# Kernel tuning notes

Hardware: AMD Instinct MI355X
Metric: run time of the kernel (lower is better)

Reference implementation:

```python
import jax, jax.numpy as jnp
import numpy as np
from math import pi

# Layer dims for num_inputs=0, width=64, depth=5, num_outputs=3
CHANNELS = [4, 64, 64, 64, 64, 3]

def _splits():
    biases, weights, idx = [], [], 0
    for l in range(len(CHANNELS) - 1):
        nci, nco = CHANNELS[l], CHANNELS[l + 1]
        biases.append((idx, idx + nco)); idx += nco
        weights.append((idx, idx + nci * nco)); idx += nci * nco
    return biases, weights, idx

BIASES, WEIGHTS, NUM_PARAMS = _splits()  # NUM_PARAMS == 12995


def _get_coords(h, w, ds):
    """Faithful port of _get_coords, including the original's bug where the
    y-channels reuse the normalized x coordinate vector (requires h == w)."""
    scale = 7.0 / 8.0
    x = jnp.arange(w, dtype=jnp.float32)
    y = jnp.arange(h, dtype=jnp.float32)
    x_c = (jnp.remainder(x, ds) / ds)
    y_c = (jnp.remainder(y, ds) / ds)
    x_c = x_c / (x_c.max() / scale)          # x_cos == x_sin in original
    y_cn = x_c / (y_c.max() / scale)          # bug: built from x_c
    xcos = jnp.cos(2.0 * pi * x_c)
    xsin = jnp.sin(2.0 * pi * x_c)
    ycos = jnp.cos(2.0 * pi * y_cn)           # length w, laid out along h (h==w)
    ysin = jnp.sin(2.0 * pi * y_cn)
    row = lambda v: jnp.broadcast_to(v[None, :], (h, w))
    col = lambda v: jnp.broadcast_to(v[:, None], (h, w))
    return jnp.stack([row(xcos), row(xsin), col(ycos), col(ysin)], axis=0)  # (4,h,w)


def setup_inputs() -> dict:
    key = jax.random.key(0)
    k1, k2 = jax.random.split(key)
    highres = jax.random.normal(k1, (2, 4, 512, 512), dtype=jnp.float32)
    lr_params = jax.random.normal(k2, (2, NUM_PARAMS, 64, 64), dtype=jnp.float32)
    return {"highres": highres, "lr_params": lr_params}


def reference(highres, lr_params):
    bs, _, h, w = highres.shape
    h_lr, w_lr = lr_params.shape[2], lr_params.shape[3]
    k = h // h_lr  # tile size

    coords = _get_coords(h, w, k)                       # (4, h, w)
    pe = jnp.broadcast_to(coords[None], (bs, 4, h, w))  # highres is overwritten by PE

    # unfold into (bs, h_lr, w_lr, k*k, 4) tiles
    tiles = pe.reshape(bs, 4, h_lr, k, w_lr, k)
    tiles = tiles.transpose(0, 2, 4, 3, 5, 1).reshape(bs, h_lr, w_lr, k * k, 4)

    out = tiles
    num_layers = len(CHANNELS) - 1
    for idx in range(num_layers):
        nci, nco = CHANNELS[idx], CHANNELS[idx + 1]
        b0, b1 = BIASES[idx]
        w0, w1 = WEIGHTS[idx]
        w_ = lr_params[:, w0:w1].transpose(0, 2, 3, 1).reshape(bs, h_lr, w_lr, nci, nco)
        b_ = lr_params[:, b0:b1].transpose(0, 2, 3, 1)[:, :, :, None, :]  # (bs,h_lr,w_lr,1,nco)
        out = jnp.einsum('bhwpi,bhwio->bhwpo', out, w_) + b_
        if idx < num_layers - 1:
            out = jnp.where(out >= 0, out, 0.01 * out)  # leaky_relu(0.01)
        else:
            out = jnp.tanh(out)

    out = out.reshape(bs, h_lr, w_lr, k, k, CHANNELS[-1])
    out = out.transpose(0, 5, 1, 3, 2, 4).reshape(bs, CHANNELS[-1], h, w)
    return out
```

## Files before the change

kernel.cpp:

```cpp
#include <hip/hip_runtime.h>
#include <math.h>


static constexpr int PLANE = 4096;
static constexpr int NPAR  = 12995;
static constexpr int AHI   = 8192;

__device__ __forceinline__ float leaky(float v) { return fmaxf(v, 0.01f * v); }

__device__ __forceinline__ constexpr float cx(int k) {
  constexpr float R = 0.70710678118654752f;
  const float t[8] = {1.f, R, 0.f, -R, -1.f, -R, 0.f, R};
  return t[k];
}
__device__ __forceinline__ constexpr float sx(int k) {
  constexpr float R = 0.70710678118654752f;
  const float t[8] = {0.f, R, 1.f, R, 0.f, -R, -1.f, -R};
  return t[k];
}

__global__ __launch_bounds__(256, 1) void pqn(const float* __restrict__ lr,
                                              float* __restrict__ out) {
  __shared__ alignas(16) float A[2 * AHI];
  __shared__ alignas(16) float WB[2][2048];

  const int tid = threadIdx.x;
  const int j   = tid & 3;
  const int pg  = (tid >> 2) & 7;
  const int cob = tid >> 5;

  const int n  = blockIdx.x;
  const int e2 = (n >> 3) & 3;
  const int P  = (n & 7) | ((n >> 5) << 3);
  const int jg = ((P & 3) << 2) | e2;
  const int i  = (P >> 2) & 63;
  const int b  = (P >> 8) & 1;

  const float* __restrict__ wb =
      lr + (size_t)b * NPAR * PLANE + (size_t)(i * 64 + jg * 4);
  const float* __restrict__ pt = wb + j;

  float fyc, fys;
  sincosf(0.78539816339744830962f * pg, &fys, &fyc);

  const int abase = pg * 16 + j * 4;
  const int swz   = j * 4;
  const int wr0   = (cob * 8) ^ swz;
  const int sq    = tid >> 7;
  const int sc    = tid & 127;

  auto gaddr = [&](int g) -> size_t {
    return 384 + (size_t)(g >> 3) * 4160 + (size_t)(g & 7) * 512;
  };

  float4 paA, paB, pbA, pbB;
  {
    const size_t cb = gaddr(0);
    paA = *(const float4*)(wb + (cb + tid) * PLANE);
    paB = *(const float4*)(wb + (cb + 256 + tid) * PLANE);
  }
  float l0b[8], l0w[32], bb[8];
#pragma unroll
  for (int m = 0; m < 8; ++m) l0b[m] = pt[(size_t)(cob * 8 + m) * PLANE];
#pragma unroll
  for (int f = 0; f < 4; ++f)
#pragma unroll
    for (int m = 0; m < 8; ++m)
      l0w[f * 8 + m] = pt[(size_t)(64 + f * 64 + cob * 8 + m) * PLANE];
#pragma unroll
  for (int m = 0; m < 8; ++m) bb[m] = pt[(size_t)(320 + cob * 8 + m) * PLANE];

#pragma unroll
  for (int col = 0; col < 8; ++col) {
    float t[8];
#pragma unroll
    for (int k = 0; k < 8; ++k) {
      float v = l0b[col];
      v = fmaf(cx(k), l0w[col], v);
      v = fmaf(sx(k), l0w[8 + col], v);
      v = fmaf(fyc,  l0w[16 + col], v);
      v = fmaf(fys,  l0w[24 + col], v);
      t[k] = leaky(v);
    }
    float4 v0, v1;
    v0.x = t[0]; v0.y = t[1]; v0.z = t[2]; v0.w = t[3];
    v1.x = t[4]; v1.y = t[5]; v1.z = t[6]; v1.w = t[7];
    *(float4*)&A[(cob * 8 + col) * 128 + abase]       = v0;
    *(float4*)&A[(cob * 8 + col) * 128 + abase + AHI] = v1;
  }
#pragma unroll
  for (int jj = 0; jj < 4; ++jj) {
    WB[0][sq * 512       + jj * 128 + (sc ^ (jj * 4))] = ((const float*)&paA)[jj];
    WB[0][(2 + sq) * 512 + jj * 128 + (sc ^ (jj * 4))] = ((const float*)&paB)[jj];
  }
  {
    size_t cb = gaddr(1);
    paA = *(const float4*)(wb + (cb + tid) * PLANE);
    paB = *(const float4*)(wb + (cb + 256 + tid) * PLANE);
    cb = gaddr(2);
    pbA = *(const float4*)(wb + (cb + tid) * PLANE);
    pbB = *(const float4*)(wb + (cb + 256 + tid) * PLANE);
  }
  asm volatile("s_waitcnt lgkmcnt(0)" ::: "memory");
  __builtin_amdgcn_s_barrier();
  __builtin_amdgcn_sched_barrier(0);

  float y[64];
#pragma unroll
  for (int m = 0; m < 64; ++m) y[m] = 0.f;

  auto cgrp = [&](int g, int h) {
    const int r0 = (g & 7) * 8;
#pragma unroll
    for (int q = 0; q < 4; ++q) {
      const float* Wt = &WB[h][q * 512 + j * 128];
#pragma unroll
      for (int cl = 0; cl < 2; ++cl) {
        const int ci = r0 + q * 2 + cl;
        const float4 a0 = *(const float4*)&A[ci * 128 + abase];
        const float4 a1 = *(const float4*)&A[ci * 128 + abase + AHI];
        const float4 w0 = *(const float4*)&Wt[(cl * 64) + wr0];
        const float4 w1 = *(const float4*)&Wt[((cl * 64 + cob * 8 + 4) ^ swz)];
        const float av[8] = {a0.x, a0.y, a0.z, a0.w, a1.x, a1.y, a1.z, a1.w};
        const float wv[8] = {w0.x, w0.y, w0.z, w0.w, w1.x, w1.y, w1.z, w1.w};
#pragma unroll
        for (int col = 0; col < 8; ++col)
#pragma unroll
          for (int k = 0; k < 8; ++k)
            y[col * 8 + k] = fmaf(av[k], wv[col], y[col * 8 + k]);
      }
    }
  };
  auto flush = [&](int l) {
#pragma unroll
    for (int col = 0; col < 8; ++col) {
      float4 v0, v1;
      v0.x = leaky(y[col * 8 + 0] + bb[col]);
      v0.y = leaky(y[col * 8 + 1] + bb[col]);
      v0.z = leaky(y[col * 8 + 2] + bb[col]);
      v0.w = leaky(y[col * 8 + 3] + bb[col]);
      v1.x = leaky(y[col * 8 + 4] + bb[col]);
      v1.y = leaky(y[col * 8 + 5] + bb[col]);
      v1.z = leaky(y[col * 8 + 6] + bb[col]);
      v1.w = leaky(y[col * 8 + 7] + bb[col]);
      *(float4*)&A[(cob * 8 + col) * 128 + abase]       = v0;
      *(float4*)&A[(cob * 8 + col) * 128 + abase + AHI] = v1;
    }
#pragma unroll
    for (int m = 0; m < 64; ++m) y[m] = 0.f;
    if (l < 2) {
#pragma unroll
      for (int m = 0; m < 8; ++m)
        bb[m] = pt[(size_t)(320 + (l + 1) * 4160 + cob * 8 + m) * PLANE];
    }
  };

#pragma unroll 1
  for (int u = 0; u < 12; ++u) {
    const int g0 = u * 2;
#pragma unroll
    for (int jj = 0; jj < 4; ++jj) {
      WB[1][sq * 512       + jj * 128 + (sc ^ (jj * 4))] = ((const float*)&paA)[jj];
      WB[1][(2 + sq) * 512 + jj * 128 + (sc ^ (jj * 4))] = ((const float*)&paB)[jj];
    }
    if (g0 + 3 < 24) {
      const size_t cb = gaddr(g0 + 3);
      paA = *(const float4*)(wb + (cb + tid) * PLANE);
      paB = *(const float4*)(wb + (cb + 256 + tid) * PLANE);
    }
    cgrp(g0, 0);
    asm volatile("s_waitcnt lgkmcnt(0)" ::: "memory");
    __builtin_amdgcn_s_barrier();
    __builtin_amdgcn_sched_barrier(0);

    const int g1 = g0 + 1;
    if (g1 + 1 < 24) {
#pragma unroll
      for (int jj = 0; jj < 4; ++jj) {
        WB[0][sq * 512       + jj * 128 + (sc ^ (jj * 4))] = ((const float*)&pbA)[jj];
        WB[0][(2 + sq) * 512 + jj * 128 + (sc ^ (jj * 4))] = ((const float*)&pbB)[jj];
      }
    }
    if (g1 + 3 < 24) {
      const size_t cb = gaddr(g1 + 3);
      pbA = *(const float4*)(wb + (cb + tid) * PLANE);
      pbB = *(const float4*)(wb + (cb + 256 + tid) * PLANE);
    }
    cgrp(g1, 1);
    asm volatile("s_waitcnt lgkmcnt(0)" ::: "memory");
    __builtin_amdgcn_s_barrier();
    __builtin_amdgcn_sched_barrier(0);
    if ((g1 & 7) == 7) {
      flush(g1 >> 3);
      asm volatile("s_waitcnt lgkmcnt(0)" ::: "memory");
      __builtin_amdgcn_s_barrier();
      __builtin_amdgcn_sched_barrier(0);
    }
  }

  float po[24];
#pragma unroll
  for (int m = 0; m < 24; ++m) po[m] = 0.f;
#pragma unroll
  for (int cl = 0; cl < 8; ++cl) {
    const int ci = cob * 8 + cl;
    const float4 a0 = *(const float4*)&A[ci * 128 + abase];
    const float4 a1 = *(const float4*)&A[ci * 128 + abase + AHI];
#pragma unroll
    for (int o = 0; o < 3; ++o) {
      const float w = pt[(size_t)(12803 + ci * 3 + o) * PLANE];
      po[o * 8 + 0] = fmaf(a0.x, w, po[o * 8 + 0]);
      po[o * 8 + 1] = fmaf(a0.y, w, po[o * 8 + 1]);
      po[o * 8 + 2] = fmaf(a0.z, w, po[o * 8 + 2]);
      po[o * 8 + 3] = fmaf(a0.w, w, po[o * 8 + 3]);
      po[o * 8 + 4] = fmaf(a1.x, w, po[o * 8 + 4]);
      po[o * 8 + 5] = fmaf(a1.y, w, po[o * 8 + 5]);
      po[o * 8 + 6] = fmaf(a1.z, w, po[o * 8 + 6]);
      po[o * 8 + 7] = fmaf(a1.w, w, po[o * 8 + 7]);
    }
  }
  asm volatile("s_waitcnt lgkmcnt(0)" ::: "memory");
  __builtin_amdgcn_s_barrier();
  float* R = A;
#pragma unroll
  for (int m = 0; m < 24; m += 4)
    *(float4*)&R[tid * 28 + m] = *(float4*)&po[m];
  asm volatile("s_waitcnt lgkmcnt(0)" ::: "memory");
  __builtin_amdgcn_s_barrier();
  __builtin_amdgcn_sched_barrier(0);

  if (cob == 0) {
#pragma unroll
    for (int o = 0; o < 3; ++o) {
      const float bias = pt[(size_t)(12800 + o) * PLANE];
      float s[8];
#pragma unroll
      for (int k = 0; k < 8; ++k) s[k] = bias;
#pragma unroll
      for (int cb = 0; cb < 8; ++cb) {
#pragma unroll
        for (int k = 0; k < 8; ++k)
          s[k] += R[(cb * 32 + tid) * 28 + o * 8 + k];
      }
      float4 v0, v1;
      v0.x = tanhf(s[0]); v0.y = tanhf(s[1]); v0.z = tanhf(s[2]); v0.w = tanhf(s[3]);
      v1.x = tanhf(s[4]); v1.y = tanhf(s[5]); v1.z = tanhf(s[6]); v1.w = tanhf(s[7]);
      float* op = out + (size_t)b * 786432 + (size_t)o * 262144 +
                  (size_t)(i * 8 + pg) * 512 + (size_t)((jg * 4 + j) * 8);
      *(float4*)op = v0;
      *(float4*)(op + 4) = v1;
    }
  }
}

extern "C" void kernel_launch(void* const* d_in, const int* in_sizes, int n_in,
                              void* d_out, int out_size, void* d_ws, size_t ws_size,
                              hipStream_t stream) {
  (void)in_sizes; (void)n_in; (void)d_ws; (void)ws_size; (void)out_size;
  const float* lr = (const float*)d_in[1];
  float* out = (float*)d_out;
  hipLaunchKernelGGL(pqn, dim3(2048), dim3(256), 0, stream, lr, out);
}
```

Before: 249.2 us.

## Software-pipeline LDS reads in inner GEMM and shorten global prefetch depth

The inner per-group compute loop now loads the next A and W float4 values from shared memory while doing the FMAs for the current ones, so LDS latency overlaps with arithmetic. The global weight prefetch drops from two register sets (three groups ahead) to one set (two groups ahead), which frees 8 VGPRs to pay for the extra prefetch registers. The cost is less slack to hide global load latency.

```diff
diff --git a/kernel.cpp b/kernel.cpp
--- a/kernel.cpp
+++ b/kernel.cpp
@@ -45,7 +45,6 @@
 
   const int abase = pg * 16 + j * 4;
   const int swz   = j * 4;
-  const int wr0   = (cob * 8) ^ swz;
   const int sq    = tid >> 7;
   const int sc    = tid & 127;
 
@@ -53,7 +52,7 @@
     return 384 + (size_t)(g >> 3) * 4160 + (size_t)(g & 7) * 512;
   };
 
-  float4 paA, paB, pbA, pbB;
+  float4 paA, paB;
   {
     const size_t cb = gaddr(0);
     paA = *(const float4*)(wb + (cb + tid) * PLANE);
@@ -94,12 +93,9 @@
     WB[0][(2 + sq) * 512 + jj * 128 + (sc ^ (jj * 4))] = ((const float*)&paB)[jj];
   }
   {
-    size_t cb = gaddr(1);
+    const size_t cb = gaddr(1);
     paA = *(const float4*)(wb + (cb + tid) * PLANE);
     paB = *(const float4*)(wb + (cb + 256 + tid) * PLANE);
-    cb = gaddr(2);
-    pbA = *(const float4*)(wb + (cb + tid) * PLANE);
-    pbB = *(const float4*)(wb + (cb + 256 + tid) * PLANE);
   }
   asm volatile("s_waitcnt lgkmcnt(0)" ::: "memory");
   __builtin_amdgcn_s_barrier();
@@ -110,25 +106,32 @@
   for (int m = 0; m < 64; ++m) y[m] = 0.f;
 
   auto cgrp = [&](int g, int h) {
+    const float* WH = WB[h];
     const int r0 = (g & 7) * 8;
-#pragma unroll
-    for (int q = 0; q < 4; ++q) {
-      const float* Wt = &WB[h][q * 512 + j * 128];
-#pragma unroll
-      for (int cl = 0; cl < 2; ++cl) {
-        const int ci = r0 + q * 2 + cl;
-        const float4 a0 = *(const float4*)&A[ci * 128 + abase];
-        const float4 a1 = *(const float4*)&A[ci * 128 + abase + AHI];
-        const float4 w0 = *(const float4*)&Wt[(cl * 64) + wr0];
-        const float4 w1 = *(const float4*)&Wt[((cl * 64 + cob * 8 + 4) ^ swz)];
-        const float av[8] = {a0.x, a0.y, a0.z, a0.w, a1.x, a1.y, a1.z, a1.w};
-        const float wv[8] = {w0.x, w0.y, w0.z, w0.w, w1.x, w1.y, w1.z, w1.w};
-#pragma unroll
-        for (int col = 0; col < 8; ++col)
-#pragma unroll
-          for (int k = 0; k < 8; ++k)
-            y[col * 8 + k] = fmaf(av[k], wv[col], y[col * 8 + k]);
+    float4 a0 = *(const float4*)&A[r0 * 128 + abase];
+    float4 a1 = *(const float4*)&A[r0 * 128 + abase + AHI];
+    float4 w0 = *(const float4*)&WH[j * 128 + ((cob * 8) ^ swz)];
+    float4 w1 = *(const float4*)&WH[j * 128 + ((cob * 8 + 4) ^ swz)];
+#pragma unroll
+    for (int t = 0; t < 8; ++t) {
+      float4 na0, na1, nw0, nw1;
+      if (t < 7) {
+        const int tn = t + 1;
+        const int ci = r0 + tn;
+        const int q = tn >> 1, cl = tn & 1;
+        na0 = *(const float4*)&A[ci * 128 + abase];
+        na1 = *(const float4*)&A[ci * 128 + abase + AHI];
+        nw0 = *(const float4*)&WH[q * 512 + j * 128 + ((cl * 64 + cob * 8) ^ swz)];
+        nw1 = *(const float4*)&WH[q * 512 + j * 128 + ((cl * 64 + cob * 8 + 4) ^ swz)];
       }
+      const float av[8] = {a0.x, a0.y, a0.z, a0.w, a1.x, a1.y, a1.z, a1.w};
+      const float wv[8] = {w0.x, w0.y, w0.z, w0.w, w1.x, w1.y, w1.z, w1.w};
+#pragma unroll
+      for (int col = 0; col < 8; ++col)
+#pragma unroll
+        for (int k = 0; k < 8; ++k)
+          y[col * 8 + k] = fmaf(av[k], wv[col], y[col * 8 + k]);
+      if (t < 7) { a0 = na0; a1 = na1; w0 = nw0; w1 = nw1; }
     }
   };
   auto flush = [&](int l) {
@@ -163,8 +166,8 @@
       WB[1][sq * 512       + jj * 128 + (sc ^ (jj * 4))] = ((const float*)&paA)[jj];
       WB[1][(2 + sq) * 512 + jj * 128 + (sc ^ (jj * 4))] = ((const float*)&paB)[jj];
     }
-    if (g0 + 3 < 24) {
-      const size_t cb = gaddr(g0 + 3);
+    if (g0 + 2 < 24) {
+      const size_t cb = gaddr(g0 + 2);
       paA = *(const float4*)(wb + (cb + tid) * PLANE);
       paB = *(const float4*)(wb + (cb + 256 + tid) * PLANE);
     }
@@ -177,14 +180,14 @@
     if (g1 + 1 < 24) {
 #pragma unroll
       for (int jj = 0; jj < 4; ++jj) {
-        WB[0][sq * 512       + jj * 128 + (sc ^ (jj * 4))] = ((const float*)&pbA)[jj];
-        WB[0][(2 + sq) * 512 + jj * 128 + (sc ^ (jj * 4))] = ((const float*)&pbB)[jj];
+        WB[0][sq * 512       + jj * 128 + (sc ^ (jj * 4))] = ((const float*)&paA)[jj];
+        WB[0][(2 + sq) * 512 + jj * 128 + (sc ^ (jj * 4))] = ((const float*)&paB)[jj];
       }
     }
-    if (g1 + 3 < 24) {
-      const size_t cb = gaddr(g1 + 3);
-      pbA = *(const float4*)(wb + (cb + tid) * PLANE);
-      pbB = *(const float4*)(wb + (cb + 256 + tid) * PLANE);
+    if (g1 + 2 < 24) {
+      const size_t cb = gaddr(g1 + 2);
+      paA = *(const float4*)(wb + (cb + tid) * PLANE);
+      paB = *(const float4*)(wb + (cb + 256 + tid) * PLANE);
     }
     cgrp(g1, 1);
     asm volatile("s_waitcnt lgkmcnt(0)" ::: "memory");
```

New measurement: 245.6 us. About the same (-1.5%).
